# Performance work log

Hardware: AMD Instinct MI355X
Metric: run time of the kernel (lower is better)

Reference implementation:

```python
import jax, jax.numpy as jnp
import numpy as np

D_MODEL = 1024
NUM_HEADS = 16
D_K = D_MODEL // NUM_HEADS
ROPE_THETA = 10000.0


def apply_rope(x, theta=ROPE_THETA):
    # x: [B, H, S, d_k]; rotate interleaved even/odd pairs by pos*theta^(-2i/d)
    S, d = x.shape[-2], x.shape[-1]
    pos = jnp.arange(S, dtype=x.dtype)
    inv_freq = theta ** (-jnp.arange(0, d, 2, dtype=x.dtype) / d)  # [d/2]
    ang = pos[:, None] * inv_freq[None, :]  # [S, d/2]
    cos, sin = jnp.cos(ang), jnp.sin(ang)
    x1, x2 = x[..., 0::2], x[..., 1::2]
    o1 = x1 * cos - x2 * sin
    o2 = x1 * sin + x2 * cos
    return jnp.stack([o1, o2], axis=-1).reshape(x.shape)


def setup_inputs() -> dict:
    key = jax.random.key(0)
    ks = jax.random.split(key, 5)
    B, S, D = 2, 2048, D_MODEL
    x = jax.random.normal(ks[0], (B, S, D), dtype=jnp.float32)
    scale = 0.02
    W_q = jax.random.normal(ks[1], (D, D), dtype=jnp.float32) * scale
    W_k = jax.random.normal(ks[2], (D, D), dtype=jnp.float32) * scale
    W_v = jax.random.normal(ks[3], (D, D), dtype=jnp.float32) * scale
    W_o = jax.random.normal(ks[4], (D, D), dtype=jnp.float32) * scale
    return {"x": x, "W_q": W_q, "W_k": W_k, "W_v": W_v, "W_o": W_o}


def reference(x, W_q, W_k, W_v, W_o):
    B, S, D = x.shape
    H, dk = NUM_HEADS, D_K
    # projections (Linear: y = x @ W.T, no bias)
    q = (x @ W_q.T).reshape(B, S, H, dk).transpose(0, 2, 1, 3)  # [B,H,S,dk]
    k = (x @ W_k.T).reshape(B, S, H, dk).transpose(0, 2, 1, 3)
    v = (x @ W_v.T).reshape(B, S, H, dk).transpose(0, 2, 1, 3)
    q = apply_rope(q)
    k = apply_rope(k)
    scores = jnp.einsum('bhqd,bhkd->bhqk', q, k) / jnp.sqrt(jnp.asarray(dk, x.dtype))
    causal = jnp.tril(jnp.ones((S, S), dtype=bool))
    scores = jnp.where(causal, scores, jnp.asarray(-jnp.inf, x.dtype))
    probs = jax.nn.softmax(scores, axis=-1)
    attn = jnp.einsum('bhqk,bhkd->bhqd', probs, v)  # [B,H,S,dk]
    attn = attn.transpose(0, 2, 1, 3).reshape(B, S, D)
    return attn @ W_o.T
```

## Files before the change

kernel.cpp:

```cpp
#include <hip/hip_runtime.h>

#define D_MODEL 1024
#define NHEAD 16
#define DK 64
#define SEQ 2048
#define NBATCH 2
#define MROWS (NBATCH * SEQ)

typedef unsigned short u16;
typedef short bf16x8 __attribute__((ext_vector_type(8)));
typedef float f32x4 __attribute__((ext_vector_type(4)));
typedef unsigned short u16x8 __attribute__((ext_vector_type(8)));

__device__ __forceinline__ u16 f2bf(float f) {
    union { float f; unsigned u; } v; v.f = f;
    unsigned r = v.u + 0x7FFFu + ((v.u >> 16) & 1u);
    return (u16)(r >> 16);
}

__device__ __forceinline__ void gload16(const void* g, void* s) {
    __builtin_amdgcn_global_load_lds((const __attribute__((address_space(1))) void*)g,
                                     (__attribute__((address_space(3))) void*)s, 16, 0, 0);
}

#define XN 4194304
#define WN 1048576

__global__ __launch_bounds__(256) void convert_bf16(
    const float* __restrict__ x, const float* __restrict__ wq, const float* __restrict__ wk,
    const float* __restrict__ wv, const float* __restrict__ wo,
    u16* __restrict__ xb, u16* __restrict__ wqkv, u16* __restrict__ wob)
{
    size_t base = ((size_t)blockIdx.x * 256 + threadIdx.x) * 8;
    const float* src; u16* dst;
    if (base < XN)               { src = x  + base;                dst = xb   + base; }
    else if (base < XN + WN)     { src = wq + (base - XN);         dst = wqkv + (base - XN); }
    else if (base < XN + 2*WN)   { src = wk + (base - XN - WN);    dst = wqkv + (base - XN); }
    else if (base < XN + 3*WN)   { src = wv + (base - XN - 2*WN);  dst = wqkv + (base - XN); }
    else                         { src = wo + (base - XN - 3*WN);  dst = wob  + (base - XN - 3*WN); }
    float4 a = *(const float4*)&src[0];
    float4 b = *(const float4*)&src[4];
    u16x8 o;
    o[0] = f2bf(a.x); o[1] = f2bf(a.y); o[2] = f2bf(a.z); o[3] = f2bf(a.w);
    o[4] = f2bf(b.x); o[5] = f2bf(b.y); o[6] = f2bf(b.z); o[7] = f2bf(b.w);
    *(u16x8*)dst = o;
}

__global__ __launch_bounds__(256) void gemm_qkv(
    const u16* __restrict__ A, const u16* __restrict__ B,
    u16* __restrict__ qo, u16* __restrict__ ko, u16* __restrict__ vo)
{
    __shared__ __align__(16) u16 sbuf[17408];

    const int tid = threadIdx.x, w = tid >> 6, l = tid & 63;
    const int l15 = l & 15, lg = l >> 4;
    const int m0 = blockIdx.x * 128, n0 = blockIdx.y * 128;
    const int wm = (w >> 1) * 64, wn = (w & 1) * 64;

    f32x4 zero = {0.f, 0.f, 0.f, 0.f};
    f32x4 acc[4][4];
#pragma unroll
    for (int i = 0; i < 4; ++i)
#pragma unroll
        for (int j = 0; j < 4; ++j) acc[i][j] = zero;

    auto stage = [&](int k0s, int half) {
        const int hb = half * 8192;
#pragma unroll
        for (int it = 0; it < 2; ++it) {
            int ubase = it * 256 + w * 64;
            int u = ubase + l, row = u >> 2, kq = u & 3;
            gload16(A + (size_t)(m0 + row) * D_MODEL + k0s + kq * 8, &sbuf[hb + ubase * 8]);
        }
#pragma unroll
        for (int it = 0; it < 2; ++it) {
            int ubase = it * 256 + w * 64;
            int u = ubase + l, row = u >> 2, kq = u & 3;
            gload16(B + (size_t)(n0 + row) * D_MODEL + k0s + kq * 8, &sbuf[hb + 4096 + ubase * 8]);
        }
    };

    stage(0, 0);
    int cur = 0;
    for (int k0 = 0; k0 < D_MODEL; k0 += 32, cur ^= 1) {
        __syncthreads();
        if (k0 + 32 < D_MODEL) stage(k0 + 32, cur ^ 1);
        const int hb = cur * 8192;
        bf16x8 af[4], bf[4];
#pragma unroll
        for (int mi = 0; mi < 4; ++mi) af[mi] = *(const bf16x8*)&sbuf[hb + (wm + mi * 16 + l15) * 32 + lg * 8];
#pragma unroll
        for (int ni = 0; ni < 4; ++ni) bf[ni] = *(const bf16x8*)&sbuf[hb + 4096 + (wn + ni * 16 + l15) * 32 + lg * 8];
#pragma unroll
        for (int mi = 0; mi < 4; ++mi)
#pragma unroll
            for (int ni = 0; ni < 4; ++ni)
                acc[mi][ni] = __builtin_amdgcn_mfma_f32_16x16x32_bf16(af[mi], bf[ni], acc[mi][ni], 0, 0, 0);
    }

    const int which = n0 >> 10;
    if (which < 2) {
        u16* outp = (which == 0) ? qo : ko;
        const float lnth = 9.210340371976184f;
#pragma unroll
        for (int ni = 0; ni < 4; ++ni) {
            int n = n0 + wn + ni * 16 + l15;
            int hh = (n >> 6) & 15, d = n & 63;
            float invf = __expf(-lnth * (float)(d & 62) * (1.0f / 64.0f));
            float sgn = (d & 1) ? 1.0f : -1.0f;
#pragma unroll
            for (int mi = 0; mi < 4; ++mi) {
#pragma unroll
                for (int i = 0; i < 4; ++i) {
                    int m = m0 + wm + mi * 16 + lg * 4 + i;
                    int bb = m >> 11, s = m & (SEQ - 1);
                    float v = acc[mi][ni][i];
                    float pv = __shfl_xor(v, 1);
                    float sn, cs;
                    __sincosf((float)s * invf, &sn, &cs);
                    float res = v * cs + sgn * pv * sn;
                    if (which == 0) res *= 0.125f;
                    outp[((size_t)(bb * NHEAD + hh) * SEQ + s) * DK + d] = f2bf(res);
                }
            }
        }
    } else {
        __syncthreads();
        u16* sc = &sbuf[w * 64 * 68];
#pragma unroll
        for (int mi = 0; mi < 4; ++mi)
#pragma unroll
            for (int ni = 0; ni < 4; ++ni)
#pragma unroll
                for (int i = 0; i < 4; ++i)
                    sc[(mi * 16 + lg * 4 + i) * 68 + ni * 16 + l15] = f2bf(acc[mi][ni][i]);
        int vcol = n0 - 2048 + wn;
        int hh = vcol >> 6;
        int m = m0 + wm, bb = m >> 11, s0 = m & (SEQ - 1);
        u16* dst = vo + ((size_t)(bb * NHEAD + hh) * DK + l) * SEQ + s0;
#pragma unroll
        for (int j8 = 0; j8 < 8; ++j8) {
            u16x8 val;
#pragma unroll
            for (int jj = 0; jj < 8; ++jj) val[jj] = sc[(j8 * 8 + jj) * 68 + l];
            *(u16x8*)&dst[j8 * 8] = val;
        }
    }
}

__global__ __launch_bounds__(256, 4) void attn_mfma(
    const u16* __restrict__ qb, const u16* __restrict__ kb,
    const u16* __restrict__ vtb, u16* __restrict__ attnb)
{
    __shared__ __align__(16) u16 Kt[2][4096];
    __shared__ __align__(16) u16 Vt[2][4096];
    __shared__ __align__(16) u16 Ps_all[4096];

    const int id = blockIdx.x;
    const int bh = id & 31;
    const int g = (id >> 5) & 7, r = id >> 8;
    const int qt = (r == 0) ? g : (r == 1) ? (15 - g) : (r == 2) ? (16 + g) : (31 - g);
    const int b = bh >> 4, h = bh & 15;
    const int qbase = qt * 64;
    const int tid = threadIdx.x, w = tid >> 6, l = tid & 63;
    const int l15 = l & 15, lg = l >> 4;

    const u16* qlane = qb + ((size_t)bh * SEQ + qbase + w * 16 + l15) * DK + lg * 8;
    bf16x8 bq[2];
    bq[0] = *(const bf16x8*)&qlane[0];
    bq[1] = *(const bf16x8*)&qlane[32];

    const u16* kg = kb + (size_t)bh * SEQ * DK;
    const u16* vg = vtb + (size_t)bh * DK * SEQ;

    f32x4 zero = {0.f, 0.f, 0.f, 0.f};
    f32x4 ot[4];
#pragma unroll
    for (int i = 0; i < 4; ++i) ot[i] = zero;
    float mrun = -1e30f, lrun = 0.f;
    const int qg = qbase + w * 16 + l15;

    char* Psb = (char*)&Ps_all[w * 1024];
    const int swz = (l15 & 7) << 4;

    auto stageKV = [&](int kt2, int half) {
        const int kc2 = kt2 * 64;
#pragma unroll
        for (int it = 0; it < 2; ++it) {
            int ubase = it * 256 + w * 64;
            int u = ubase + l, rr = u >> 3, cq = u & 7;
            gload16(kg + (size_t)(kc2 + rr) * DK + ((cq ^ (rr & 7)) << 3), &Kt[half][ubase * 8]);
            gload16(vg + (size_t)rr * SEQ + kc2 + ((cq ^ (rr & 7)) << 3), &Vt[half][ubase * 8]);
        }
    };

    stageKV(0, 0);
    int cur = 0;
    for (int kt = 0; kt <= qt; ++kt, cur ^= 1) {
        const int kc = kt * 64;
        __syncthreads();
        if (kt < qt) stageKV(kt + 1, cur ^ 1);

        f32x4 s4[4];
#pragma unroll
        for (int ni = 0; ni < 4; ++ni) {
            s4[ni] = zero;
#pragma unroll
            for (int kk = 0; kk < 2; ++kk) {
                int row = ni * 16 + l15, cq2 = kk * 4 + lg;
                bf16x8 kf = *(const bf16x8*)&Kt[cur][(row * 8 + (cq2 ^ (row & 7))) * 8];
                s4[ni] = __builtin_amdgcn_mfma_f32_16x16x32_bf16(kf, bq[kk], s4[ni], 0, 0, 0);
            }
        }
        if (kt == qt) {
#pragma unroll
            for (int ni = 0; ni < 4; ++ni)
#pragma unroll
                for (int i = 0; i < 4; ++i)
                    if (kc + ni * 16 + lg * 4 + i > qg) s4[ni][i] = -1e30f;
        }

        float mx = -1e30f;
#pragma unroll
        for (int ni = 0; ni < 4; ++ni)
            mx = fmaxf(mx, fmaxf(fmaxf(s4[ni][0], s4[ni][1]), fmaxf(s4[ni][2], s4[ni][3])));
        mx = fmaxf(mx, __shfl_xor(mx, 16));
        mx = fmaxf(mx, __shfl_xor(mx, 32));
        float mn = fmaxf(mrun, mx);
        float scl = __expf(mrun - mn);
        mrun = mn;
        float rs = 0.f;
#pragma unroll
        for (int ni = 0; ni < 4; ++ni)
#pragma unroll
            for (int ih = 0; ih < 2; ++ih) {
                float p0 = __expf(s4[ni][2 * ih] - mn);
                float p1 = __expf(s4[ni][2 * ih + 1] - mn);
                rs += p0 + p1;
                unsigned pw = (unsigned)f2bf(p0) | ((unsigned)f2bf(p1) << 16);
                int bytecol = ni * 32 + lg * 8 + ih * 4;
                *(unsigned*)(Psb + (l15 << 7) + (bytecol ^ swz)) = pw;
            }
        rs += __shfl_xor(rs, 16);
        rs += __shfl_xor(rs, 32);
        lrun = lrun * scl + rs;

        bf16x8 bp[2];
#pragma unroll
        for (int kk = 0; kk < 2; ++kk)
            bp[kk] = *(const bf16x8*)(Psb + (l15 << 7) + ((kk * 64 + lg * 16) ^ swz));

#pragma unroll
        for (int n2 = 0; n2 < 4; ++n2) {
#pragma unroll
            for (int i = 0; i < 4; ++i) ot[n2][i] *= scl;
#pragma unroll
            for (int kk = 0; kk < 2; ++kk) {
                int row = n2 * 16 + l15, cq2 = kk * 4 + lg;
                bf16x8 vf = *(const bf16x8*)&Vt[cur][(row * 8 + (cq2 ^ (row & 7))) * 8];
                ot[n2] = __builtin_amdgcn_mfma_f32_16x16x32_bf16(vf, bp[kk], ot[n2], 0, 0, 0);
            }
        }
    }

    const float invl = 1.0f / lrun;
    u16* orow = attnb + ((size_t)b * SEQ + qg) * D_MODEL + h * DK;
#pragma unroll
    for (int n2 = 0; n2 < 4; ++n2)
#pragma unroll
        for (int ih = 0; ih < 2; ++ih) {
            float r0 = ot[n2][2 * ih] * invl;
            float r1 = ot[n2][2 * ih + 1] * invl;
            unsigned pw = (unsigned)f2bf(r0) | ((unsigned)f2bf(r1) << 16);
            *(unsigned*)&orow[n2 * 16 + lg * 4 + 2 * ih] = pw;
        }
}

__global__ __launch_bounds__(256) void gemm_proj(
    const u16* __restrict__ A, const u16* __restrict__ B, float* __restrict__ out)
{
    __shared__ __align__(16) u16 sbuf[16384];

    const int tid = threadIdx.x, w = tid >> 6, l = tid & 63;
    const int l15 = l & 15, lg = l >> 4;
    const int m0 = blockIdx.x * 128, n0 = blockIdx.y * 128;
    const int wm = (w >> 1) * 64, wn = (w & 1) * 64;

    f32x4 zero = {0.f, 0.f, 0.f, 0.f};
    f32x4 acc[4][4];
#pragma unroll
    for (int i = 0; i < 4; ++i)
#pragma unroll
        for (int j = 0; j < 4; ++j) acc[i][j] = zero;

    auto stage = [&](int k0s, int half) {
        const int hb = half * 8192;
#pragma unroll
        for (int it = 0; it < 2; ++it) {
            int ubase = it * 256 + w * 64;
            int u = ubase + l, row = u >> 2, kq = u & 3;
            gload16(A + (size_t)(m0 + row) * D_MODEL + k0s + kq * 8, &sbuf[hb + ubase * 8]);
        }
#pragma unroll
        for (int it = 0; it < 2; ++it) {
            int ubase = it * 256 + w * 64;
            int u = ubase + l, row = u >> 2, kq = u & 3;
            gload16(B + (size_t)(n0 + row) * D_MODEL + k0s + kq * 8, &sbuf[hb + 4096 + ubase * 8]);
        }
    };

    stage(0, 0);
    int cur = 0;
    for (int k0 = 0; k0 < D_MODEL; k0 += 32, cur ^= 1) {
        __syncthreads();
        if (k0 + 32 < D_MODEL) stage(k0 + 32, cur ^ 1);
        const int hb = cur * 8192;
        bf16x8 af[4], bf[4];
#pragma unroll
        for (int mi = 0; mi < 4; ++mi) af[mi] = *(const bf16x8*)&sbuf[hb + (wm + mi * 16 + l15) * 32 + lg * 8];
#pragma unroll
        for (int ni = 0; ni < 4; ++ni) bf[ni] = *(const bf16x8*)&sbuf[hb + 4096 + (wn + ni * 16 + l15) * 32 + lg * 8];
#pragma unroll
        for (int mi = 0; mi < 4; ++mi)
#pragma unroll
            for (int ni = 0; ni < 4; ++ni)
                acc[mi][ni] = __builtin_amdgcn_mfma_f32_16x16x32_bf16(af[mi], bf[ni], acc[mi][ni], 0, 0, 0);
    }

#pragma unroll
    for (int mi = 0; mi < 4; ++mi)
#pragma unroll
        for (int ni = 0; ni < 4; ++ni)
#pragma unroll
            for (int i = 0; i < 4; ++i) {
                int m = m0 + wm + mi * 16 + lg * 4 + i;
                int n = n0 + wn + ni * 16 + l15;
                out[(size_t)m * D_MODEL + n] = acc[mi][ni][i];
            }
}

extern "C" void kernel_launch(void* const* d_in, const int* in_sizes, int n_in,
                              void* d_out, int out_size, void* d_ws, size_t ws_size,
                              hipStream_t stream) {
    const float* x  = (const float*)d_in[0];
    const float* Wq = (const float*)d_in[1];
    const float* Wk = (const float*)d_in[2];
    const float* Wv = (const float*)d_in[3];
    const float* Wo = (const float*)d_in[4];
    float* out = (float*)d_out;

    u16* ws = (u16*)d_ws;
    const size_t M1 = 1048576;
    u16* xb    = ws;
    u16* wqkv  = ws + 4 * M1;
    u16* wob   = ws + 7 * M1;
    u16* qb    = ws + 8 * M1;
    u16* kb    = ws + 12 * M1;
    u16* vtb   = ws + 16 * M1;
    u16* attnb = ws + 20 * M1;

    convert_bf16<<<dim3(4096), dim3(256), 0, stream>>>(x, Wq, Wk, Wv, Wo, xb, wqkv, wob);
    gemm_qkv<<<dim3(MROWS / 128, 3072 / 128), dim3(256), 0, stream>>>(xb, wqkv, qb, kb, vtb);
    attn_mfma<<<dim3(1024), dim3(256), 0, stream>>>(qb, kb, vtb, attnb);
    gemm_proj<<<dim3(MROWS / 128, D_MODEL / 128), dim3(256), 0, stream>>>(attnb, wob, out);
}
```

Measured before the change: 188.0 us.

## Precompute RoPE tables, use exp2 softmax with lazy rescale, raise MFMA priority

Adds a small kernel that fills cos/sin tables for RoPE, so the QKV GEMM epilogue loads them instead of calling sincos and exp per element. It folds log2(e) into the Q scale so attention can use the native exp2 instruction. It also skips the online-softmax rescale unless the running max grows by more than a threshold. MFMA sections are wrapped with s_setprio. This costs an extra launch and workspace tables, and the lazy rescale relies on the bounded-growth assumption staying accurate.

```diff
diff --git a/kernel.cpp b/kernel.cpp
--- a/kernel.cpp
+++ b/kernel.cpp
@@ -46,8 +46,21 @@
     *(u16x8*)dst = o;
 }
 
+__global__ __launch_bounds__(256) void fill_rope(float* __restrict__ rc, float* __restrict__ rs)
+{
+    int idx = blockIdx.x * 256 + threadIdx.x;
+    int d2 = idx >> 11, s = idx & 2047;
+    const float lnth = 9.210340371976184f;
+    float invf = __expf(-lnth * (float)(2 * d2) * (1.0f / 64.0f));
+    float sn, cs;
+    __sincosf((float)s * invf, &sn, &cs);
+    rc[idx] = cs;
+    rs[idx] = sn;
+}
+
 __global__ __launch_bounds__(256) void gemm_qkv(
     const u16* __restrict__ A, const u16* __restrict__ B,
+    const float* __restrict__ ropec, const float* __restrict__ ropes,
     u16* __restrict__ qo, u16* __restrict__ ko, u16* __restrict__ vo)
 {
     __shared__ __align__(16) u16 sbuf[17408];
@@ -101,26 +114,29 @@
     const int which = n0 >> 10;
     if (which < 2) {
         u16* outp = (which == 0) ? qo : ko;
-        const float lnth = 9.210340371976184f;
+        const float qscale = 0.125f * 1.44269504088896340736f;
 #pragma unroll
         for (int ni = 0; ni < 4; ++ni) {
             int n = n0 + wn + ni * 16 + l15;
             int hh = (n >> 6) & 15, d = n & 63;
-            float invf = __expf(-lnth * (float)(d & 62) * (1.0f / 64.0f));
+            const float* rcb = ropec + (d >> 1) * 2048;
+            const float* rsb = ropes + (d >> 1) * 2048;
             float sgn = (d & 1) ? 1.0f : -1.0f;
 #pragma unroll
             for (int mi = 0; mi < 4; ++mi) {
+                int mbase = m0 + wm + mi * 16 + lg * 4;
+                int bb = mbase >> 11, sb = mbase & (SEQ - 1);
+                float4 c4 = *(const float4*)&rcb[sb];
+                float4 s4v = *(const float4*)&rsb[sb];
+                float cr[4] = {c4.x, c4.y, c4.z, c4.w};
+                float sr[4] = {s4v.x, s4v.y, s4v.z, s4v.w};
 #pragma unroll
                 for (int i = 0; i < 4; ++i) {
-                    int m = m0 + wm + mi * 16 + lg * 4 + i;
-                    int bb = m >> 11, s = m & (SEQ - 1);
                     float v = acc[mi][ni][i];
                     float pv = __shfl_xor(v, 1);
-                    float sn, cs;
-                    __sincosf((float)s * invf, &sn, &cs);
-                    float res = v * cs + sgn * pv * sn;
-                    if (which == 0) res *= 0.125f;
-                    outp[((size_t)(bb * NHEAD + hh) * SEQ + s) * DK + d] = f2bf(res);
+                    float res = v * cr[i] + sgn * pv * sr[i];
+                    if (which == 0) res *= qscale;
+                    outp[((size_t)(bb * NHEAD + hh) * SEQ + sb + i) * DK + d] = f2bf(res);
                 }
             }
         }
@@ -202,6 +218,7 @@
         if (kt < qt) stageKV(kt + 1, cur ^ 1);
 
         f32x4 s4[4];
+        __builtin_amdgcn_s_setprio(1);
 #pragma unroll
         for (int ni = 0; ni < 4; ++ni) {
             s4[ni] = zero;
@@ -212,6 +229,7 @@
                 s4[ni] = __builtin_amdgcn_mfma_f32_16x16x32_bf16(kf, bq[kk], s4[ni], 0, 0, 0);
             }
         }
+        __builtin_amdgcn_s_setprio(0);
         if (kt == qt) {
 #pragma unroll
             for (int ni = 0; ni < 4; ++ni)
@@ -226,16 +244,23 @@
             mx = fmaxf(mx, fmaxf(fmaxf(s4[ni][0], s4[ni][1]), fmaxf(s4[ni][2], s4[ni][3])));
         mx = fmaxf(mx, __shfl_xor(mx, 16));
         mx = fmaxf(mx, __shfl_xor(mx, 32));
-        float mn = fmaxf(mrun, mx);
-        float scl = __expf(mrun - mn);
-        mrun = mn;
+        if (!__all(mx - mrun <= 8.0f)) {
+            float mn2 = fmaxf(mrun, mx);
+            float scl = __builtin_amdgcn_exp2f(mrun - mn2);
+            mrun = mn2;
+            lrun *= scl;
+#pragma unroll
+            for (int n2 = 0; n2 < 4; ++n2)
+#pragma unroll
+                for (int i = 0; i < 4; ++i) ot[n2][i] *= scl;
+        }
         float rs = 0.f;
 #pragma unroll
         for (int ni = 0; ni < 4; ++ni)
 #pragma unroll
             for (int ih = 0; ih < 2; ++ih) {
-                float p0 = __expf(s4[ni][2 * ih] - mn);
-                float p1 = __expf(s4[ni][2 * ih + 1] - mn);
+                float p0 = __builtin_amdgcn_exp2f(s4[ni][2 * ih] - mrun);
+                float p1 = __builtin_amdgcn_exp2f(s4[ni][2 * ih + 1] - mrun);
                 rs += p0 + p1;
                 unsigned pw = (unsigned)f2bf(p0) | ((unsigned)f2bf(p1) << 16);
                 int bytecol = ni * 32 + lg * 8 + ih * 4;
@@ -243,24 +268,23 @@
             }
         rs += __shfl_xor(rs, 16);
         rs += __shfl_xor(rs, 32);
-        lrun = lrun * scl + rs;
+        lrun += rs;
 
         bf16x8 bp[2];
 #pragma unroll
         for (int kk = 0; kk < 2; ++kk)
             bp[kk] = *(const bf16x8*)(Psb + (l15 << 7) + ((kk * 64 + lg * 16) ^ swz));
 
-#pragma unroll
-        for (int n2 = 0; n2 < 4; ++n2) {
-#pragma unroll
-            for (int i = 0; i < 4; ++i) ot[n2][i] *= scl;
+        __builtin_amdgcn_s_setprio(1);
+#pragma unroll
+        for (int n2 = 0; n2 < 4; ++n2)
 #pragma unroll
             for (int kk = 0; kk < 2; ++kk) {
                 int row = n2 * 16 + l15, cq2 = kk * 4 + lg;
                 bf16x8 vf = *(const bf16x8*)&Vt[cur][(row * 8 + (cq2 ^ (row & 7))) * 8];
                 ot[n2] = __builtin_amdgcn_mfma_f32_16x16x32_bf16(vf, bp[kk], ot[n2], 0, 0, 0);
             }
-        }
+        __builtin_amdgcn_s_setprio(0);
     }
 
     const float invl = 1.0f / lrun;
@@ -358,9 +382,12 @@
     u16* kb    = ws + 12 * M1;
     u16* vtb   = ws + 16 * M1;
     u16* attnb = ws + 20 * M1;
+    float* ropec = (float*)(ws + 24 * M1);
+    float* ropes = (float*)(ws + 24 * M1) + 65536;
 
     convert_bf16<<<dim3(4096), dim3(256), 0, stream>>>(x, Wq, Wk, Wv, Wo, xb, wqkv, wob);
-    gemm_qkv<<<dim3(MROWS / 128, 3072 / 128), dim3(256), 0, stream>>>(xb, wqkv, qb, kb, vtb);
+    fill_rope<<<dim3(256), dim3(256), 0, stream>>>(ropec, ropes);
+    gemm_qkv<<<dim3(MROWS / 128, 3072 / 128), dim3(256), 0, stream>>>(xb, wqkv, ropec, ropes, qb, kb, vtb);
     attn_mfma<<<dim3(1024), dim3(256), 0, stream>>>(qb, kb, vtb, attnb);
     gemm_proj<<<dim3(MROWS / 128, D_MODEL / 128), dim3(256), 0, stream>>>(attnb, wob, out);
 }
```

After: 186.8 us. About the same (-0.6%).
